# Performance work log

Hardware: AMD Instinct MI355X
Metric: run time of the kernel (lower is better)

The kernel has to match this reference:

```python
import jax, jax.numpy as jnp
import numpy as np

MEM_DIM = 128  # GRU hidden / memory dim
EMB_DIM = 512  # encoder embedding dim (jk_out_channels)
N_ACTIVE = 200000
MAX_NODES = 250000
OUT_CH = 2


def setup_inputs() -> dict:
    key = jax.random.key(0)
    ks = jax.random.split(key, 8)
    s_ih = 1.0 / np.sqrt(MEM_DIM)
    return {
        "embeddings": jax.random.normal(ks[0], (N_ACTIVE, EMB_DIM), jnp.float32),
        "node_ids": jnp.arange(N_ACTIVE, dtype=jnp.int64 if jax.config.jax_enable_x64 else jnp.int32),
        "memory_bank": jax.random.normal(ks[1], (MAX_NODES, MEM_DIM), jnp.float32),
        "W_ih": jax.random.uniform(ks[2], (3 * MEM_DIM, EMB_DIM), jnp.float32, -s_ih, s_ih),
        "W_hh": jax.random.uniform(ks[3], (3 * MEM_DIM, MEM_DIM), jnp.float32, -s_ih, s_ih),
        "b_ih": jax.random.uniform(ks[4], (3 * MEM_DIM,), jnp.float32, -s_ih, s_ih),
        "b_hh": jax.random.uniform(ks[5], (3 * MEM_DIM,), jnp.float32, -s_ih, s_ih),
        "W_cls": jax.random.uniform(ks[6], (OUT_CH, EMB_DIM + MEM_DIM), jnp.float32, -1.0 / np.sqrt(EMB_DIM + MEM_DIM), 1.0 / np.sqrt(EMB_DIM + MEM_DIM)),
        "b_cls": jax.random.uniform(ks[7], (OUT_CH,), jnp.float32, -1.0 / np.sqrt(EMB_DIM + MEM_DIM), 1.0 / np.sqrt(EMB_DIM + MEM_DIM)),
    }


def gru_cell(x, h, W_ih, W_hh, b_ih, b_hh):
    # torch.nn.GRUCell math. x: [N, E], h: [N, M]
    gi = x @ W_ih.T + b_ih                 # [N, 3M]
    gh = h @ W_hh.T + b_hh                 # [N, 3M]
    i_r, i_z, i_n = jnp.split(gi, 3, axis=1)
    h_r, h_z, h_n = jnp.split(gh, 3, axis=1)
    r = jax.nn.sigmoid(i_r + h_r)
    z = jax.nn.sigmoid(i_z + h_z)
    n = jnp.tanh(i_n + r * h_n)
    return (1.0 - z) * n + z * h


def reference(embeddings, node_ids, memory_bank, W_ih, W_hh, b_ih, b_hh, W_cls, b_cls):
    # gather per-node memory
    prev_mem = memory_bank[node_ids]                       # [N, M]
    # GRUCell update
    new_mem = gru_cell(embeddings, prev_mem, W_ih, W_hh, b_ih, b_hh)
    # scatter back (detached in the original)
    updated_bank = memory_bank.at[node_ids].set(jax.lax.stop_gradient(new_mem))
    # concat + linear classify (dropout is identity at eval)
    combined = jnp.concatenate([embeddings, new_mem], axis=1)  # [N, E+M]
    logits = combined @ W_cls.T + b_cls                        # [N, out]
    return logits, updated_bank
```

## Files before the change

### kernel.cpp

```cpp
#include <hip/hip_runtime.h>
#include <hip/hip_bf16.h>

typedef short short8 __attribute__((ext_vector_type(8)));
typedef float f32x4  __attribute__((ext_vector_type(4)));
typedef float f32x16 __attribute__((ext_vector_type(16)));

#define EMB   512
#define MEM   128
#define G3    384
#define CLS_K 640
#define KJ    640
#define NKS   20
#define ROWS  64
#define NTHR  512
#define WB_CLS (G3 * KJ)

#define OFF_A    0
#define OFF_B    16384
#define OFF_CLS  65536
#define OFF_CLSM 67584
#define OFF_ELP  68608
#define SMEM_SZ  69120

__device__ __forceinline__ short f2b(float f) {
  __hip_bfloat16 h = __float2bfloat16(f);
  return __builtin_bit_cast(short, h);
}
__device__ __forceinline__ float b2f(short s) {
  return __uint_as_float(((unsigned)(unsigned short)s) << 16);
}
__device__ __forceinline__ short8 cvt8(f32x4 a, f32x4 b) {
  short8 v;
  v[0] = f2b(a[0]); v[1] = f2b(a[1]); v[2] = f2b(a[2]); v[3] = f2b(a[3]);
  v[4] = f2b(b[0]); v[5] = f2b(b[1]); v[6] = f2b(b[2]); v[7] = f2b(b[3]);
  return v;
}
__device__ __forceinline__ float sigm(float x)     { return 1.f / (1.f + __expf(-x)); }
__device__ __forceinline__ float tanhfast(float x) { return 2.f / (1.f + __expf(-2.f * x)) - 1.f; }

__device__ __forceinline__ void gll16(const void* gsrc, void* ldst) {
  __builtin_amdgcn_global_load_lds(
      (const __attribute__((address_space(1))) unsigned int*)gsrc,
      (__attribute__((address_space(3))) unsigned int*)ldst, 16, 0, 0);
}

__global__ void prep_w_kernel(const float* __restrict__ wih, const float* __restrict__ whh,
                              const float* __restrict__ wcls, short* __restrict__ outw) {
  int i = blockIdx.x * blockDim.x + threadIdx.x;
  const int nJ = G3 * KJ;
  const int nTot = nJ + 2 * EMB;
  if (i < nJ) {
    const int e  = i & 7;
    const int cc = (i >> 3) % 1536;
    const int kc = (i >> 3) / 1536;
    const int col = cc % G3;
    const int kq  = cc / G3;
    const int k = kc * 32 + kq * 8 + e;
    const float v = (k < EMB) ? wih[(size_t)col * EMB + k] : whh[(size_t)col * MEM + (k - EMB)];
    outw[i] = f2b(v);
  } else if (i < nTot) {
    const int j = i - nJ;
    const int r = j >> 9, k = j & 511;
    outw[i] = f2b(wcls[(size_t)r * CLS_K + k]);
  }
}

__global__ void bitmap_set_kernel(const int* __restrict__ ids, unsigned char* __restrict__ bm, int n) {
  int i = blockIdx.x * blockDim.x + threadIdx.x;
  if (i < n) bm[ids[i]] = 1;
}

__global__ void copy_bank_kernel(const f32x4* __restrict__ src, f32x4* __restrict__ dst,
                                 const unsigned char* __restrict__ bm, int n4) {
  int i = blockIdx.x * blockDim.x + threadIdx.x;
  int stride = gridDim.x * blockDim.x;
  for (; i < n4; i += stride) {
    if (bm && bm[i >> 5]) continue;
    dst[i] = src[i];
  }
}

template <bool ASYNC>
__global__ __launch_bounds__(NTHR, 4)
void fused_gru_kernel(const float* __restrict__ emb, const int* __restrict__ ids,
                      const float* __restrict__ bank,
                      const float* __restrict__ Wihf, const float* __restrict__ Whhf,
                      const float* __restrict__ bih,  const float* __restrict__ bhh,
                      const float* __restrict__ Wcls, const float* __restrict__ bcls,
                      const short* __restrict__ Wb,
                      float* __restrict__ out_logits, float* __restrict__ out_bank, int N) {
  __shared__ __align__(16) char smem[SMEM_SZ];

  const int t   = threadIdx.x;
  const int l   = t & 63;
  const int w   = t >> 6;
  const int wr  = w >> 2;
  const int wc  = w & 3;
  const int lk2 = l >> 5;
  const int l31 = l & 31;
  const int r0  = blockIdx.x * ROWS;

  int growE = r0 + l; if (growE > N - 1) growE = N - 1;
  const int gidE0 = ids[growE];

  const int rowS = w * 8 + (l >> 3);
  const int chS  = (l & 7) ^ ((l >> 3) & 7);
  int growS = r0 + rowS; if (growS > N - 1) growS = N - 1;
  const int gidS = ids[growS];
  const float* pEmbRow  = emb  + (size_t)growS * EMB + chS * 4;
  const float* pBankRow = bank + (size_t)gidS  * MEM + chS * 4;

  if (t < 128) {
    short8 v;
    if constexpr (ASYNC) v = *(const short8*)(Wb + WB_CLS + t * 8);
    else {
      const int r = t >> 6, k = (t & 63) * 8;
      const float* p = Wcls + (size_t)r * CLS_K + k;
      v = cvt8(*(const f32x4*)p, *(const f32x4*)(p + 4));
    }
    *(short8*)(smem + OFF_CLS + t * 16) = v;
  } else if (t < 384) {
    const int i = t - 128;
    const int r = i >> 7, m = i & 127;
    ((float*)(smem + OFF_CLSM))[r * 128 + m] = Wcls[(size_t)r * CLS_K + EMB + m];
  }

  const int mcol = wc * 32 + l31;
  const float birv = bih[mcol] + bhh[mcol];
  const float bizv = bih[MEM + mcol] + bhh[MEM + mcol];
  const float binv = bih[2 * MEM + mcol];
  const float bhnv = bhh[2 * MEM + mcol];

  auto STAGE = [&](int kc) {
    const int buf = kc & 1;
    const float* srcA = (kc < 16) ? (pEmbRow + kc * 32) : (pBankRow + (kc - 16) * 32);
    gll16(srcA, smem + OFF_A + buf * 8192 + w * 1024);
    if constexpr (ASYNC) {
      const short* wbk = Wb + (size_t)kc * 12288;
#pragma unroll
      for (int s = 0; s < 3; ++s)
        gll16(wbk + (s * 512 + w * 64 + l) * 8,
              smem + OFF_B + buf * 24576 + (s * 512 + w * 64) * 16);
    } else {
#pragma unroll
      for (int s = 0; s < 3; ++s) {
        const int g = s * 512 + w * 64 + l;
        const int col = g % G3, kq = g / G3;
        const int k = kc * 32 + kq * 8;
        const float* p = (k < EMB) ? (Wihf + (size_t)col * EMB + k)
                                   : (Whhf + (size_t)col * MEM + (k - EMB));
        short8 v = cvt8(*(const f32x4*)p, *(const f32x4*)(p + 4));
        *(short8*)(smem + OFF_B + buf * 24576 + g * 16) = v;
      }
    }
  };

  STAGE(0);
  __syncthreads();

  f32x16 accR = {}, accZ = {}, accIN = {}, accHN = {};
  float clsL0 = 0.f, clsL1 = 0.f;

  const int arow = wr * 32 + l31;
  const int aswz = arow & 7;
  const int bOffC = lk2 * 6144 + (wc * 32 + l31) * 16;

  for (int kc = 0; kc < NKS; ++kc) {
    const int buf = kc & 1;
    if (kc + 1 < NKS) STAGE(kc + 1);

    const char* ap = smem + OFF_A + buf * 8192 + arow * 128;
    const char* bp = smem + OFF_B + buf * 24576;
#pragma unroll
    for (int ks = 0; ks < 2; ++ks) {
      const int c0 = ks * 4 + lk2 * 2;
      const f32x4 av0 = *(const f32x4*)(ap + ((c0 ^ aswz) << 4));
      const f32x4 av1 = *(const f32x4*)(ap + (((c0 + 1) ^ aswz) << 4));
      const short8 af = cvt8(av0, av1);
      if (wc == 0 && kc < 16) {
        const short8 w0 = *(const short8*)(smem + OFF_CLS + kc * 64 + ks * 32 + lk2 * 16);
        const short8 w1 = *(const short8*)(smem + OFF_CLS + 1024 + kc * 64 + ks * 32 + lk2 * 16);
#pragma unroll
        for (int i = 0; i < 4; ++i) {
          clsL0 += av0[i] * b2f(w0[i]) + av1[i] * b2f(w0[i + 4]);
          clsL1 += av0[i] * b2f(w1[i]) + av1[i] * b2f(w1[i + 4]);
        }
      }
      const short8 b0 = *(const short8*)(bp + bOffC + ks * 12288);
      const short8 b1 = *(const short8*)(bp + bOffC + ks * 12288 + 2048);
      const short8 b2 = *(const short8*)(bp + bOffC + ks * 12288 + 4096);
      accR = __builtin_amdgcn_mfma_f32_32x32x16_bf16(af, b0, accR, 0, 0, 0);
      accZ = __builtin_amdgcn_mfma_f32_32x32x16_bf16(af, b1, accZ, 0, 0, 0);
      if (kc < 16) accIN = __builtin_amdgcn_mfma_f32_32x32x16_bf16(af, b2, accIN, 0, 0, 0);
      else         accHN = __builtin_amdgcn_mfma_f32_32x32x16_bf16(af, b2, accHN, 0, 0, 0);
    }
    __syncthreads();
  }

  float* nvT = (float*)smem;
  float hp[16];
#pragma unroll
  for (int j = 0; j < 16; ++j) {
    const int row32 = (j & 3) + 8 * (j >> 2) + 4 * lk2;
    const int gid = __shfl(gidE0, wr * 32 + row32);
    hp[j] = bank[(size_t)gid * MEM + mcol];
  }
#pragma unroll
  for (int j = 0; j < 16; ++j) {
    const int row32 = (j & 3) + 8 * (j >> 2) + 4 * lk2;
    const int row = wr * 32 + row32;
    const float rg = sigm(accR[j] + birv);
    const float zg = sigm(accZ[j] + bizv);
    const float ng = tanhfast(accIN[j] + binv + rg * (accHN[j] + bhnv));
    nvT[row * 132 + mcol] = (1.f - zg) * ng + zg * hp[j];
  }
  if (wc == 0) {
    const float e0 = clsL0 + __shfl_xor(clsL0, 32);
    const float e1 = clsL1 + __shfl_xor(clsL1, 32);
    if (l < 32) {
      float* elp = (float*)(smem + OFF_ELP);
      elp[(wr * 32 + l) * 2 + 0] = e0;
      elp[(wr * 32 + l) * 2 + 1] = e1;
    }
  }
  __syncthreads();

  {
    const int row = t >> 3, q = t & 7;
    const int gid = __shfl(gidE0, row);
    const f32x4 v0 = *(const f32x4*)(nvT + row * 132 + q * 16);
    const f32x4 v1 = *(const f32x4*)(nvT + row * 132 + q * 16 + 4);
    const f32x4 v2 = *(const f32x4*)(nvT + row * 132 + q * 16 + 8);
    const f32x4 v3 = *(const f32x4*)(nvT + row * 132 + q * 16 + 12);
    float* dst = out_bank + (size_t)gid * MEM + q * 16;
    *(f32x4*)dst = v0; *(f32x4*)(dst + 4) = v1; *(f32x4*)(dst + 8) = v2; *(f32x4*)(dst + 12) = v3;

    const float* cm0 = (const float*)(smem + OFF_CLSM) + q * 16;
    const float* cm1 = (const float*)(smem + OFF_CLSM) + 128 + q * 16;
    float lp0 = 0.f, lp1 = 0.f;
#pragma unroll
    for (int i = 0; i < 4; ++i) {
      lp0 += v0[i] * cm0[i] + v1[i] * cm0[4 + i] + v2[i] * cm0[8 + i] + v3[i] * cm0[12 + i];
      lp1 += v0[i] * cm1[i] + v1[i] * cm1[4 + i] + v2[i] * cm1[8 + i] + v3[i] * cm1[12 + i];
    }
#pragma unroll
    for (int s = 1; s < 8; s <<= 1) { lp0 += __shfl_xor(lp0, s); lp1 += __shfl_xor(lp1, s); }
    if (q == 0 && r0 + row < N) {
      const float* elp = (const float*)(smem + OFF_ELP);
      out_logits[(size_t)(r0 + row) * 2 + 0] = lp0 + elp[row * 2 + 0] + bcls[0];
      out_logits[(size_t)(r0 + row) * 2 + 1] = lp1 + elp[row * 2 + 1] + bcls[1];
    }
  }
}

extern "C" void kernel_launch(void* const* d_in, const int* in_sizes, int n_in,
                              void* d_out, int out_size, void* d_ws, size_t ws_size,
                              hipStream_t stream) {
  const float* emb  = (const float*)d_in[0];
  const int*   ids  = (const int*)d_in[1];
  const float* bank = (const float*)d_in[2];
  const float* wih  = (const float*)d_in[3];
  const float* whh  = (const float*)d_in[4];
  const float* bih  = (const float*)d_in[5];
  const float* bhh  = (const float*)d_in[6];
  const float* wcls = (const float*)d_in[7];
  const float* bcls = (const float*)d_in[8];

  const int N          = in_sizes[1];
  const int bank_elems = in_sizes[2];
  const int bank_rows  = bank_elems / MEM;
  const int n4         = bank_elems / 4;

  float* out_logits = (float*)d_out;
  float* out_bank   = (float*)d_out + (size_t)N * 2;

  const int wtot = G3 * KJ + 2 * EMB;
  const size_t wbytes  = (size_t)wtot * sizeof(short);
  const size_t bmbytes = ((size_t)bank_rows + 15) & ~15ull;

  const bool haveW  = ws_size >= wbytes;
  const bool haveBM = ws_size >= wbytes + bmbytes;

  short* wb = (short*)d_ws;
  unsigned char* bm = (unsigned char*)d_ws + wbytes;

  if (haveW)
    prep_w_kernel<<<(wtot + 255) / 256, 256, 0, stream>>>(wih, whh, wcls, wb);

  const int nb = (N + ROWS - 1) / ROWS;
  if (haveW)
    fused_gru_kernel<true><<<nb, NTHR, 0, stream>>>(emb, ids, bank, wih, whh, bih, bhh,
                                                    wcls, bcls, wb, out_logits, out_bank, N);
  else
    fused_gru_kernel<false><<<nb, NTHR, 0, stream>>>(emb, ids, bank, wih, whh, bih, bhh,
                                                     wcls, bcls, nullptr, out_logits, out_bank, N);

  if (haveBM) {
    hipMemsetAsync(bm, 0, bmbytes, stream);
    bitmap_set_kernel<<<(N + 255) / 256, 256, 0, stream>>>(ids, bm, N);
    copy_bank_kernel<<<4096, 256, 0, stream>>>((const f32x4*)bank, (f32x4*)out_bank, bm, n4);
  } else {
    copy_bank_kernel<<<4096, 256, 0, stream>>>((const f32x4*)bank, (f32x4*)out_bank, nullptr, n4);
  }
}
```

Measured before the change: 261.8 us.

## Stage A tile as bf16 via register prefetch instead of async fp32 LDS loads

```diff
diff --git a/kernel.cpp b/kernel.cpp
--- a/kernel.cpp
+++ b/kernel.cpp
@@ -16,11 +16,11 @@
 #define WB_CLS (G3 * KJ)
 
 #define OFF_A    0
-#define OFF_B    16384
-#define OFF_CLS  65536
-#define OFF_CLSM 67584
-#define OFF_ELP  68608
-#define SMEM_SZ  69120
+#define OFF_B    8192
+#define OFF_CLS  57344
+#define OFF_CLSM 59392
+#define OFF_ELP  60416
+#define SMEM_SZ  60928
 
 __device__ __forceinline__ short f2b(float f) {
   __hip_bfloat16 h = __float2bfloat16(f);
@@ -103,12 +103,16 @@
   int growE = r0 + l; if (growE > N - 1) growE = N - 1;
   const int gidE0 = ids[growE];
 
-  const int rowS = w * 8 + (l >> 3);
-  const int chS  = (l & 7) ^ ((l >> 3) & 7);
-  int growS = r0 + rowS; if (growS > N - 1) growS = N - 1;
-  const int gidS = ids[growS];
-  const float* pEmbRow  = emb  + (size_t)growS * EMB + chS * 4;
-  const float* pBankRow = bank + (size_t)gidS  * MEM + chS * 4;
+  const bool stager = t < 256;
+  const int sRow = t >> 2;
+  const int sC   = t & 3;
+  int growA = r0 + sRow; if (growA > N - 1) growA = N - 1;
+  const int gidA = ids[growA];
+  const float* pEmbA  = emb  + (size_t)growA * EMB + sC * 8;
+  const float* pBankA = bank + (size_t)gidA  * MEM + sC * 8;
+  const int sSlot = sC * 64 + (sRow ^ sC);
+
+  f32x4 pa0, pa1;
 
   if (t < 128) {
     short8 v;
@@ -131,10 +135,19 @@
   const float binv = bih[2 * MEM + mcol];
   const float bhnv = bhh[2 * MEM + mcol];
 
-  auto STAGE = [&](int kc) {
+  auto A_LOAD = [&](int kc) {
+    if (stager) {
+      const float* p = (kc < 16) ? (pEmbA + kc * 32) : (pBankA + (kc - 16) * 32);
+      pa0 = *(const f32x4*)p;
+      pa1 = *(const f32x4*)(p + 4);
+    }
+  };
+  auto A_WRITE = [&](int kc) {
+    if (stager)
+      *(short8*)(smem + OFF_A + (kc & 1) * 4096 + sSlot * 16) = cvt8(pa0, pa1);
+  };
+  auto STAGE_B = [&](int kc) {
     const int buf = kc & 1;
-    const float* srcA = (kc < 16) ? (pEmbRow + kc * 32) : (pBankRow + (kc - 16) * 32);
-    gll16(srcA, smem + OFF_A + buf * 8192 + w * 1024);
     if constexpr (ASYNC) {
       const short* wbk = Wb + (size_t)kc * 12288;
 #pragma unroll
@@ -155,35 +168,35 @@
     }
   };
 
-  STAGE(0);
+  A_LOAD(0);
+  STAGE_B(0);
+  A_WRITE(0);
   __syncthreads();
 
   f32x16 accR = {}, accZ = {}, accIN = {}, accHN = {};
   float clsL0 = 0.f, clsL1 = 0.f;
 
-  const int arow = wr * 32 + l31;
-  const int aswz = arow & 7;
+  const int arow  = wr * 32 + l31;
   const int bOffC = lk2 * 6144 + (wc * 32 + l31) * 16;
 
   for (int kc = 0; kc < NKS; ++kc) {
     const int buf = kc & 1;
-    if (kc + 1 < NKS) STAGE(kc + 1);
-
-    const char* ap = smem + OFF_A + buf * 8192 + arow * 128;
+    if (kc + 1 < NKS) { A_LOAD(kc + 1); STAGE_B(kc + 1); }
+
+    const char* ap = smem + OFF_A + buf * 4096;
     const char* bp = smem + OFF_B + buf * 24576;
 #pragma unroll
     for (int ks = 0; ks < 2; ++ks) {
-      const int c0 = ks * 4 + lk2 * 2;
-      const f32x4 av0 = *(const f32x4*)(ap + ((c0 ^ aswz) << 4));
-      const f32x4 av1 = *(const f32x4*)(ap + (((c0 + 1) ^ aswz) << 4));
-      const short8 af = cvt8(av0, av1);
+      const int q = ks * 2 + lk2;
+      const short8 af = *(const short8*)(ap + (q * 64 + (arow ^ q)) * 16);
       if (wc == 0 && kc < 16) {
         const short8 w0 = *(const short8*)(smem + OFF_CLS + kc * 64 + ks * 32 + lk2 * 16);
         const short8 w1 = *(const short8*)(smem + OFF_CLS + 1024 + kc * 64 + ks * 32 + lk2 * 16);
 #pragma unroll
-        for (int i = 0; i < 4; ++i) {
-          clsL0 += av0[i] * b2f(w0[i]) + av1[i] * b2f(w0[i + 4]);
-          clsL1 += av0[i] * b2f(w1[i]) + av1[i] * b2f(w1[i + 4]);
+        for (int i = 0; i < 8; ++i) {
+          const float va = b2f(af[i]);
+          clsL0 += va * b2f(w0[i]);
+          clsL1 += va * b2f(w1[i]);
         }
       }
       const short8 b0 = *(const short8*)(bp + bOffC + ks * 12288);
@@ -194,6 +207,7 @@
       if (kc < 16) accIN = __builtin_amdgcn_mfma_f32_32x32x16_bf16(af, b2, accIN, 0, 0, 0);
       else         accHN = __builtin_amdgcn_mfma_f32_32x32x16_bf16(af, b2, accHN, 0, 0, 0);
     }
+    if (kc + 1 < NKS) A_WRITE(kc + 1);
     __syncthreads();
   }
 
```

New measurement: 279.4 us. 6.7% more time.
